# Optimization experiments

Hardware: AMD Instinct MI355X
Metric: run time of the kernel (lower is better)

## Reference

```python
import jax, jax.numpy as jnp
import numpy as np

B, O, R = 4, 1000, 20000
NF, RD, ED = 6, 1, 100
RH, OH = 150, 100


def setup_inputs() -> dict:
    key = jax.random.key(0)
    ks = jax.random.split(key, 20)
    s = 0.05
    inp = {
        "objects": jax.random.normal(ks[0], (B, O, NF), jnp.float32),
        "sender_relations": jax.random.uniform(ks[1], (B, O, R), jnp.float32),
        "receiver_relations": jax.random.uniform(ks[2], (B, O, R), jnp.float32),
        "relation_info": jax.random.normal(ks[3], (B, R, RD), jnp.float32),
        # relational MLP: (2*NF+RD) -> 150 -> 150 -> 150 -> ED, ReLU after every layer
        "rw1": jax.random.normal(ks[4], (2 * NF + RD, RH), jnp.float32) * s,
        "rb1": jnp.zeros((RH,), jnp.float32),
        "rw2": jax.random.normal(ks[5], (RH, RH), jnp.float32) * s,
        "rb2": jnp.zeros((RH,), jnp.float32),
        "rw3": jax.random.normal(ks[6], (RH, RH), jnp.float32) * s,
        "rb3": jnp.zeros((RH,), jnp.float32),
        "rw4": jax.random.normal(ks[7], (RH, ED), jnp.float32) * s,
        "rb4": jnp.zeros((ED,), jnp.float32),
        # object MLP: (NF+ED) -> 100 -> 2, ReLU only after first layer
        "ow1": jax.random.normal(ks[8], (NF + ED, OH), jnp.float32) * s,
        "ob1": jnp.zeros((OH,), jnp.float32),
        "ow2": jax.random.normal(ks[9], (OH, 2), jnp.float32) * s,
        "ob2": jnp.zeros((2,), jnp.float32),
    }
    return inp


def reference(objects, sender_relations, receiver_relations, relation_info,
              rw1, rb1, rw2, rb2, rw3, rb3, rw4, rb4,
              ow1, ob1, ow2, ob2):
    # marshalling: dense one-hot gather via bmm
    senders = jnp.einsum('bnr,bnf->brf', sender_relations, objects)    # [B,R,NF]
    receivers = jnp.einsum('bnr,bnf->brf', receiver_relations, objects)  # [B,R,NF]
    Bm = jnp.concatenate([senders, receivers, relation_info], axis=2)  # [B,R,2NF+RD]
    # relational MLP (ReLU after every layer, including the last)
    h = jax.nn.relu(Bm @ rw1 + rb1)
    h = jax.nn.relu(h @ rw2 + rb2)
    h = jax.nn.relu(h @ rw3 + rb3)
    E = jax.nn.relu(h @ rw4 + rb4)                                     # [B,R,ED]
    # aggregator: dense scatter via bmm
    effect_receivers = jnp.einsum('bnr,brf->bnf', receiver_relations, E)  # [B,O,ED]
    C = jnp.concatenate([objects, effect_receivers], axis=2)           # [B,O,NF+ED]
    # object MLP, flattened over batch*objects like the torch view(-1, input)
    Cf = C.reshape(-1, C.shape[-1])
    o = jax.nn.relu(Cf @ ow1 + ob1)
    return o @ ow2 + ob2                                               # [B*O, 2]
```

## Files before the change

kernel.cpp:

```cpp
#include <hip/hip_runtime.h>

#define B_   4
#define O_   1000
#define R_   20000
#define NF_  6
#define EDP_ 128
#define KS_  25
#define CHUNK_ 800
#define MPAD_ 1024

#define ET_OFF   2560000
#define PART_OFF 7680000
#define WT_USHORTS (4 * 2 * 25600)

typedef short bf16x8 __attribute__((ext_vector_type(8)));
typedef float f32x4  __attribute__((ext_vector_type(4)));
typedef unsigned short ushort4v __attribute__((ext_vector_type(4)));
typedef unsigned short ushort8v __attribute__((ext_vector_type(8)));

#define MFMA16 __builtin_amdgcn_mfma_f32_16x16x32_bf16

__device__ __forceinline__ unsigned short f2bf(float x) {
    union { float f; unsigned int u; } v; v.f = x;
    unsigned int r = (v.u + 0x7FFFu + ((v.u >> 16) & 1u)) >> 16;
    return (unsigned short)r;
}

__device__ __forceinline__ float bf2f(unsigned short h) {
    union { unsigned int u; float f; } v; v.u = (unsigned int)h << 16;
    return v.f;
}

__global__ __launch_bounds__(256) void k_prep(
    const float* __restrict__ rw1, const float* __restrict__ rb1,
    const float* __restrict__ rw2, const float* __restrict__ rb2,
    const float* __restrict__ rw3, const float* __restrict__ rb3,
    const float* __restrict__ rw4, const float* __restrict__ rb4,
    unsigned short* __restrict__ Wt, float* __restrict__ bfp)
{
    const int l = blockIdx.y;
    const float* Ws[4] = {rw1, rw2, rw3, rw4};
    const float* Bs[4] = {rb1, rb2, rb3, rb4};
    const int   Ksz[4] = {13, 150, 150, 150};
    const int   Nsz[4] = {150, 150, 150, 100};
    const float* w = Ws[l];
    const int K = Ksz[l], N = Nsz[l];

    int idx = blockIdx.x * 256 + threadIdx.x;
    if (idx < 25600) {
        int n = idx / 160, k = idx % 160;
        float v = (k < K && n < N) ? w[k * N + n] : 0.f;
        unsigned short h = f2bf(v);
        unsigned short lo = f2bf(v - bf2f(h));
        Wt[(size_t)l * 51200 + idx]         = h;
        Wt[(size_t)l * 51200 + 25600 + idx] = lo;
    }
    if (blockIdx.x == 0 && threadIdx.x < 160)
        bfp[l * 160 + threadIdx.x] = (threadIdx.x < (unsigned)N) ? Bs[l][threadIdx.x] : 0.f;
}

__global__ __launch_bounds__(256) void k_marshal(
    const float* __restrict__ obj, const float* __restrict__ S,
    const float* __restrict__ RRm, const float* __restrict__ rinfo,
    float* __restrict__ bmp)
{
    __shared__ float sobj[500 * NF_];
    const int b = blockIdx.y, z = blockIdx.z;
    const int n0 = z * 500;
    for (int i = threadIdx.x; i < 500 * NF_; i += 256)
        sobj[i] = obj[(size_t)b * O_ * NF_ + (size_t)n0 * NF_ + i];
    __syncthreads();

    const int r = blockIdx.x * 256 + threadIdx.x;
    if (r >= R_) return;

    const size_t base = (size_t)b * O_ * R_ + (size_t)n0 * R_ + r;
    const float* Sp = S + base;
    const float* Rp = RRm + base;

    float ss[NF_] = {0.f, 0.f, 0.f, 0.f, 0.f, 0.f};
    float rs[NF_] = {0.f, 0.f, 0.f, 0.f, 0.f, 0.f};

    #pragma unroll 4
    for (int n = 0; n < 500; ++n) {
        float sv = Sp[(size_t)n * R_];
        float rv = Rp[(size_t)n * R_];
        #pragma unroll
        for (int f = 0; f < NF_; ++f) {
            float o = sobj[n * NF_ + f];
            ss[f] = fmaf(sv, o, ss[f]);
            rs[f] = fmaf(rv, o, rs[f]);
        }
    }

    float* outp = bmp + ((size_t)z * 80000 + (size_t)b * R_ + r) * 16;
    #pragma unroll
    for (int f = 0; f < NF_; ++f) {
        outp[f]     = ss[f];
        outp[6 + f] = rs[f];
    }
    outp[12] = (z == 0) ? rinfo[(size_t)b * R_ + r] : 0.f;
}

template<int NT>
__device__ __forceinline__ void layer_mm(
    const unsigned short (*act)[168],
    const unsigned short* __restrict__ Wh, const unsigned short* __restrict__ Wl,
    int arow, int koff, int cl, f32x4* acc)
{
    #pragma unroll
    for (int n = 0; n < NT; ++n) acc[n] = (f32x4){0.f, 0.f, 0.f, 0.f};
    #pragma unroll
    for (int ks = 0; ks < 5; ++ks) {
        bf16x8 a = *(const bf16x8*)&act[arow][ks * 32 + koff];
        #pragma unroll
        for (int n = 0; n < NT; ++n) {
            bf16x8 wh = *(const bf16x8*)(Wh + (size_t)(n * 16 + cl) * 160 + ks * 32 + koff);
            bf16x8 wl = *(const bf16x8*)(Wl + (size_t)(n * 16 + cl) * 160 + ks * 32 + koff);
            acc[n] = MFMA16(a, wh, acc[n], 0, 0, 0);
            acc[n] = MFMA16(a, wl, acc[n], 0, 0, 0);
        }
    }
}

template<int NT>
__device__ __forceinline__ void epi(
    f32x4* acc, const float* __restrict__ bias,
    unsigned short (*out)[168], int m0, int cl, int rg0)
{
    __syncthreads();
    #pragma unroll
    for (int n = 0; n < NT; ++n) {
        int col = n * 16 + cl;
        float bv = bias[col];
        #pragma unroll
        for (int rg = 0; rg < 4; ++rg) {
            float v = fmaxf(acc[n][rg] + bv, 0.f);
            out[m0 + rg0 + rg][col] = f2bf(v);
        }
    }
    __syncthreads();
}

__global__ __launch_bounds__(256) void k_mlp(
    const float* __restrict__ bmp, unsigned short* __restrict__ Et,
    const unsigned short* __restrict__ Wt, const float* __restrict__ bfp)
{
    __shared__ unsigned short act[64][168];
    __shared__ unsigned short alo[64][32];
    const int t = threadIdx.x;
    const size_t row0 = (size_t)blockIdx.x * 64;

    for (int idx = t; idx < 64 * 32; idx += 256) {
        int rr = idx >> 5, k = idx & 31;
        float v = 0.f;
        if (k < 13)
            v = bmp[(row0 + rr) * 16 + k]
              + bmp[(size_t)80000 * 16 + (row0 + rr) * 16 + k];
        unsigned short h = f2bf(v);
        act[rr][k] = h;
        alo[rr][k] = f2bf(v - bf2f(h));
    }
    __syncthreads();

    const int lane = t & 63, wave = t >> 6;
    const int m0   = wave * 16;
    const int arow = m0 + (lane & 15);
    const int koff = (lane >> 4) * 8;
    const int cl   = lane & 15;
    const int rg0  = (lane >> 4) * 4;

    f32x4 acc[10];

    {
        const unsigned short* Wh = Wt;
        const unsigned short* Wl = Wt + 25600;
        bf16x8 ah = *(const bf16x8*)&act[arow][koff];
        bf16x8 al = *(const bf16x8*)&alo[arow][koff];
        #pragma unroll
        for (int n = 0; n < 10; ++n) {
            bf16x8 wh = *(const bf16x8*)(Wh + (size_t)(n * 16 + cl) * 160 + koff);
            bf16x8 wl = *(const bf16x8*)(Wl + (size_t)(n * 16 + cl) * 160 + koff);
            f32x4 a = (f32x4){0.f, 0.f, 0.f, 0.f};
            a = MFMA16(ah, wh, a, 0, 0, 0);
            a = MFMA16(ah, wl, a, 0, 0, 0);
            a = MFMA16(al, wh, a, 0, 0, 0);
            acc[n] = a;
        }
    }
    epi<10>(acc, bfp + 0 * 160, act, m0, cl, rg0);

    layer_mm<10>(act, Wt + 1 * 51200, Wt + 1 * 51200 + 25600, arow, koff, cl, acc);
    epi<10>(acc, bfp + 1 * 160, act, m0, cl, rg0);

    layer_mm<10>(act, Wt + 2 * 51200, Wt + 2 * 51200 + 25600, arow, koff, cl, acc);
    epi<10>(acc, bfp + 2 * 160, act, m0, cl, rg0);

    layer_mm<7>(act, Wt + 3 * 51200, Wt + 3 * 51200 + 25600, arow, koff, cl, acc);
    epi<7>(acc, bfp + 3 * 160, act, m0, cl, rg0);

    for (int idx = t; idx < 64 * 128; idx += 256) {
        int rr = idx & 63, j = idx >> 6;
        size_t gr = row0 + rr;
        int b = (int)(gr / R_);
        int r = (int)(gr - (size_t)b * R_);
        Et[((size_t)(b * EDP_ + j)) * R_ + r] = (j < 100) ? act[rr][j] : (unsigned short)0;
    }
}

__global__ __launch_bounds__(256) void k_agg(
    const float* __restrict__ RRm, const unsigned short* __restrict__ Et,
    float* __restrict__ part)
{
    __shared__ unsigned short sB[2][128][36];
    const int t = threadIdx.x;
    const int mt = blockIdx.x, b = blockIdx.y, kz = blockIdx.z;
    const int lane = t & 63, wave = t >> 6;
    const int k0 = kz * CHUNK_;

    const int br0 = t >> 2, bc0 = (t & 3) * 8;
    const int br1 = br0 + 64;
    const unsigned short* EtB = Et + (size_t)b * EDP_ * R_;

    int n = mt * 64 + wave * 16 + (lane & 15); if (n > 999) n = 999;
    const int cl = lane & 15, koff = (lane >> 4) * 8;
    const float* Ap = RRm + ((size_t)(b * O_) + n) * R_ + k0 + koff;

    f32x4 acc[8] = {};
    float4 a0c, a1c;
    float4 a0n = {0.f, 0.f, 0.f, 0.f}, a1n = {0.f, 0.f, 0.f, 0.f};

    {
        ushort8v v0 = *(const ushort8v*)(EtB + (size_t)br0 * R_ + k0 + bc0);
        ushort8v v1 = *(const ushort8v*)(EtB + (size_t)br1 * R_ + k0 + bc0);
        *(ushort8v*)&sB[0][br0][bc0] = v0;
        *(ushort8v*)&sB[0][br1][bc0] = v1;
        a0c = *(const float4*)(Ap + 0);
        a1c = *(const float4*)(Ap + 4);
    }
    __syncthreads();

    for (int it = 0; it < CHUNK_ / 32; ++it) {
        const int cur = it & 1, nxt = cur ^ 1;
        const bool more = (it + 1 < CHUNK_ / 32);
        ushort8v v0, v1;
        if (more) {
            const int kb = k0 + (it + 1) * 32;
            v0 = *(const ushort8v*)(EtB + (size_t)br0 * R_ + kb + bc0);
            v1 = *(const ushort8v*)(EtB + (size_t)br1 * R_ + kb + bc0);
            a0n = *(const float4*)(Ap + (it + 1) * 32);
            a1n = *(const float4*)(Ap + (it + 1) * 32 + 4);
        }
        bf16x8 af;
        af[0] = (short)f2bf(a0c.x); af[1] = (short)f2bf(a0c.y);
        af[2] = (short)f2bf(a0c.z); af[3] = (short)f2bf(a0c.w);
        af[4] = (short)f2bf(a1c.x); af[5] = (short)f2bf(a1c.y);
        af[6] = (short)f2bf(a1c.z); af[7] = (short)f2bf(a1c.w);
        #pragma unroll
        for (int ni = 0; ni < 8; ++ni) {
            bf16x8 bf = *(const bf16x8*)&sB[cur][ni * 16 + cl][koff];
            acc[ni] = MFMA16(af, bf, acc[ni], 0, 0, 0);
        }
        if (more) {
            *(ushort8v*)&sB[nxt][br0][bc0] = v0;
            *(ushort8v*)&sB[nxt][br1][bc0] = v1;
        }
        __syncthreads();
        a0c = a0n; a1c = a1n;
    }

    const int rowb = mt * 64 + wave * 16 + (lane >> 4) * 4;
    float* pp = part + ((size_t)(kz * 4 + b) * MPAD_) * 128;
    #pragma unroll
    for (int ni = 0; ni < 8; ++ni)
        #pragma unroll
        for (int rg = 0; rg < 4; ++rg)
            pp[(size_t)(rowb + rg) * 128 + ni * 16 + cl] = acc[ni][rg];
}

__global__ __launch_bounds__(256) void k_obj(
    const float* __restrict__ obj, const float* __restrict__ part,
    const float* __restrict__ ow1, const float* __restrict__ ob1,
    const float* __restrict__ ow2, const float* __restrict__ ob2,
    float* __restrict__ out)
{
    __shared__ float C[8][112];
    __shared__ float h[8][104];
    const int t = threadIdx.x;
    const int g0 = blockIdx.x * 8;

    for (int idx = t; idx < 8 * NF_; idx += 256) {
        int rr = idx / NF_, f = idx % NF_;
        C[rr][f] = obj[(size_t)(g0 + rr) * NF_ + f];
    }
    for (int idx = t; idx < 8 * 100; idx += 256) {
        int rr = idx / 100, f = idx % 100;
        int g = g0 + rr, b = g / 1000, n = g % 1000;
        float s = 0.f;
        for (int z = 0; z < KS_; ++z)
            s += part[((size_t)(z * 4 + b) * MPAD_ + n) * 128 + f];
        C[rr][6 + f] = s;
    }
    __syncthreads();

    for (int idx = t; idx < 8 * 100; idx += 256) {
        int rr = idx / 100, j = idx % 100;
        float acc = ob1[j];
        for (int k = 0; k < 106; ++k)
            acc = fmaf(C[rr][k], ow1[k * 100 + j], acc);
        h[rr][j] = fmaxf(acc, 0.f);
    }
    __syncthreads();

    if (t < 16) {
        int rr = t >> 1, j = t & 1;
        float acc = ob2[j];
        for (int k = 0; k < 100; ++k)
            acc = fmaf(h[rr][k], ow2[k * 2 + j], acc);
        out[(size_t)(g0 + rr) * 2 + j] = acc;
    }
}

extern "C" void kernel_launch(void* const* d_in, const int* in_sizes, int n_in,
                              void* d_out, int out_size, void* d_ws, size_t ws_size,
                              hipStream_t stream)
{
    const float* obj   = (const float*)d_in[0];
    const float* S     = (const float*)d_in[1];
    const float* RRm   = (const float*)d_in[2];
    const float* rinfo = (const float*)d_in[3];
    const float* rw1   = (const float*)d_in[4];
    const float* rb1   = (const float*)d_in[5];
    const float* rw2   = (const float*)d_in[6];
    const float* rb2   = (const float*)d_in[7];
    const float* rw3   = (const float*)d_in[8];
    const float* rb3   = (const float*)d_in[9];
    const float* rw4   = (const float*)d_in[10];
    const float* rb4   = (const float*)d_in[11];
    const float* ow1   = (const float*)d_in[12];
    const float* ob1   = (const float*)d_in[13];
    const float* ow2   = (const float*)d_in[14];
    const float* ob2   = (const float*)d_in[15];

    float* ws            = (float*)d_ws;
    float* bmp           = ws;
    unsigned short* Et   = (unsigned short*)(ws + ET_OFF);
    float* part          = ws + PART_OFF;
    unsigned short* Wt   = (unsigned short*)(ws + PART_OFF);
    float* bfp           = ws + PART_OFF + (WT_USHORTS / 2);
    float* out           = (float*)d_out;

    k_prep<<<dim3(100, 4), 256, 0, stream>>>(rw1, rb1, rw2, rb2, rw3, rb3, rw4, rb4,
                                             Wt, bfp);
    k_marshal<<<dim3(79, 4, 2), 256, 0, stream>>>(obj, S, RRm, rinfo, bmp);
    k_mlp<<<dim3(1250), 256, 0, stream>>>(bmp, Et, Wt, bfp);
    k_agg<<<dim3(16, 4, KS_), 256, 0, stream>>>(RRm, Et, part);
    k_obj<<<dim3(500), 256, 0, stream>>>(obj, part, ow1, ob1, ow2, ob2, out);
}
```

Baseline: 383.0 us.

## Fuse marshalling into relational MLP kernel and double M-tile in aggregation

The separate marshal kernel is removed. Each MLP block now computes its 64 relations' sender/receiver sums itself, with 4 waves each covering 250 objects and reducing through shared memory, so the intermediate bmp buffer no longer round-trips through global memory. The aggregation kernel now has each wave handle two 16-row M tiles, so every loaded E tile is reused by 128 object rows and the Et stream is read half as often. The trade-offs are that the marshal part now runs in only 1252 blocks, with coalescing limited to 64 relations per row segment. The aggregation kernel also needs more registers.

New measurement: 464.6 us. +21.3%, slower.

```diff
diff --git a/kernel.cpp b/kernel.cpp
--- a/kernel.cpp
+++ b/kernel.cpp
@@ -9,8 +9,8 @@
 #define CHUNK_ 800
 #define MPAD_ 1024
 
-#define ET_OFF   2560000
-#define PART_OFF 7680000
+#define ET_OFF   0
+#define PART_OFF 5120000
 #define WT_USHORTS (4 * 2 * 25600)
 
 typedef short bf16x8 __attribute__((ext_vector_type(8)));
@@ -59,49 +59,6 @@
         bfp[l * 160 + threadIdx.x] = (threadIdx.x < (unsigned)N) ? Bs[l][threadIdx.x] : 0.f;
 }
 
-__global__ __launch_bounds__(256) void k_marshal(
-    const float* __restrict__ obj, const float* __restrict__ S,
-    const float* __restrict__ RRm, const float* __restrict__ rinfo,
-    float* __restrict__ bmp)
-{
-    __shared__ float sobj[500 * NF_];
-    const int b = blockIdx.y, z = blockIdx.z;
-    const int n0 = z * 500;
-    for (int i = threadIdx.x; i < 500 * NF_; i += 256)
-        sobj[i] = obj[(size_t)b * O_ * NF_ + (size_t)n0 * NF_ + i];
-    __syncthreads();
-
-    const int r = blockIdx.x * 256 + threadIdx.x;
-    if (r >= R_) return;
-
-    const size_t base = (size_t)b * O_ * R_ + (size_t)n0 * R_ + r;
-    const float* Sp = S + base;
-    const float* Rp = RRm + base;
-
-    float ss[NF_] = {0.f, 0.f, 0.f, 0.f, 0.f, 0.f};
-    float rs[NF_] = {0.f, 0.f, 0.f, 0.f, 0.f, 0.f};
-
-    #pragma unroll 4
-    for (int n = 0; n < 500; ++n) {
-        float sv = Sp[(size_t)n * R_];
-        float rv = Rp[(size_t)n * R_];
-        #pragma unroll
-        for (int f = 0; f < NF_; ++f) {
-            float o = sobj[n * NF_ + f];
-            ss[f] = fmaf(sv, o, ss[f]);
-            rs[f] = fmaf(rv, o, rs[f]);
-        }
-    }
-
-    float* outp = bmp + ((size_t)z * 80000 + (size_t)b * R_ + r) * 16;
-    #pragma unroll
-    for (int f = 0; f < NF_; ++f) {
-        outp[f]     = ss[f];
-        outp[6 + f] = rs[f];
-    }
-    outp[12] = (z == 0) ? rinfo[(size_t)b * R_ + r] : 0.f;
-}
-
 template<int NT>
 __device__ __forceinline__ void layer_mm(
     const unsigned short (*act)[168],
@@ -143,20 +100,55 @@
 }
 
 __global__ __launch_bounds__(256) void k_mlp(
-    const float* __restrict__ bmp, unsigned short* __restrict__ Et,
+    const float* __restrict__ obj, const float* __restrict__ S,
+    const float* __restrict__ RRm, const float* __restrict__ rinfo,
+    unsigned short* __restrict__ Et,
     const unsigned short* __restrict__ Wt, const float* __restrict__ bfp)
 {
     __shared__ unsigned short act[64][168];
     __shared__ unsigned short alo[64][32];
-    const int t = threadIdx.x;
-    const size_t row0 = (size_t)blockIdx.x * 64;
+    __shared__ float psum[4][64][12];
+    const int t  = threadIdx.x;
+    const int b  = blockIdx.y;
+    const int r0 = blockIdx.x * 64;
+
+    {
+        const int rl = t & 63;
+        const int w  = t >> 6;
+        int rme = r0 + rl; if (rme > R_ - 1) rme = R_ - 1;
+        const float* Sp = S   + (size_t)b * O_ * R_ + (size_t)(w * 250) * R_ + rme;
+        const float* Rp = RRm + (size_t)b * O_ * R_ + (size_t)(w * 250) * R_ + rme;
+        const float* ob = obj + ((size_t)b * O_ + (size_t)(w * 250)) * NF_;
+        float ss[6] = {0.f,0.f,0.f,0.f,0.f,0.f};
+        float rs[6] = {0.f,0.f,0.f,0.f,0.f,0.f};
+        #pragma unroll 2
+        for (int n = 0; n < 250; ++n) {
+            float sv = Sp[(size_t)n * R_];
+            float rv = Rp[(size_t)n * R_];
+            #pragma unroll
+            for (int f = 0; f < 6; ++f) {
+                float o = ob[n * NF_ + f];
+                ss[f] = fmaf(sv, o, ss[f]);
+                rs[f] = fmaf(rv, o, rs[f]);
+            }
+        }
+        #pragma unroll
+        for (int f = 0; f < 6; ++f) {
+            psum[w][rl][f]     = ss[f];
+            psum[w][rl][6 + f] = rs[f];
+        }
+    }
+    __syncthreads();
 
     for (int idx = t; idx < 64 * 32; idx += 256) {
         int rr = idx >> 5, k = idx & 31;
         float v = 0.f;
-        if (k < 13)
-            v = bmp[(row0 + rr) * 16 + k]
-              + bmp[(size_t)80000 * 16 + (row0 + rr) * 16 + k];
+        if (k < 12) {
+            v = psum[0][rr][k] + psum[1][rr][k] + psum[2][rr][k] + psum[3][rr][k];
+        } else if (k == 12) {
+            int r = r0 + rr; if (r > R_ - 1) r = R_ - 1;
+            v = rinfo[(size_t)b * R_ + r];
+        }
         unsigned short h = f2bf(v);
         act[rr][k] = h;
         alo[rr][k] = f2bf(v - bf2f(h));
@@ -201,10 +193,9 @@
 
     for (int idx = t; idx < 64 * 128; idx += 256) {
         int rr = idx & 63, j = idx >> 6;
-        size_t gr = row0 + rr;
-        int b = (int)(gr / R_);
-        int r = (int)(gr - (size_t)b * R_);
-        Et[((size_t)(b * EDP_ + j)) * R_ + r] = (j < 100) ? act[rr][j] : (unsigned short)0;
+        int r = r0 + rr;
+        if (r < R_)
+            Et[((size_t)(b * EDP_ + j)) * R_ + r] = (j < 100) ? act[rr][j] : (unsigned short)0;
     }
 }
 
@@ -222,21 +213,27 @@
     const int br1 = br0 + 64;
     const unsigned short* EtB = Et + (size_t)b * EDP_ * R_;
 
-    int n = mt * 64 + wave * 16 + (lane & 15); if (n > 999) n = 999;
     const int cl = lane & 15, koff = (lane >> 4) * 8;
-    const float* Ap = RRm + ((size_t)(b * O_) + n) * R_ + k0 + koff;
-
-    f32x4 acc[8] = {};
-    float4 a0c, a1c;
-    float4 a0n = {0.f, 0.f, 0.f, 0.f}, a1n = {0.f, 0.f, 0.f, 0.f};
+    int n0 = mt * 128 + wave * 32 + cl;
+    int n1 = n0 + 16;
+    if (n0 > 999) n0 = 999;
+    if (n1 > 999) n1 = 999;
+    const float* Ap0 = RRm + ((size_t)(b * O_) + n0) * R_ + k0 + koff;
+    const float* Ap1 = RRm + ((size_t)(b * O_) + n1) * R_ + k0 + koff;
+
+    f32x4 acc[2][8] = {};
+    float4 a0c, a1c, a2c, a3c;
+    float4 a0n = {0,0,0,0}, a1n = {0,0,0,0}, a2n = {0,0,0,0}, a3n = {0,0,0,0};
 
     {
         ushort8v v0 = *(const ushort8v*)(EtB + (size_t)br0 * R_ + k0 + bc0);
         ushort8v v1 = *(const ushort8v*)(EtB + (size_t)br1 * R_ + k0 + bc0);
         *(ushort8v*)&sB[0][br0][bc0] = v0;
         *(ushort8v*)&sB[0][br1][bc0] = v1;
-        a0c = *(const float4*)(Ap + 0);
-        a1c = *(const float4*)(Ap + 4);
+        a0c = *(const float4*)(Ap0 + 0);
+        a1c = *(const float4*)(Ap0 + 4);
+        a2c = *(const float4*)(Ap1 + 0);
+        a3c = *(const float4*)(Ap1 + 4);
     }
     __syncthreads();
 
@@ -248,34 +245,44 @@
             const int kb = k0 + (it + 1) * 32;
             v0 = *(const ushort8v*)(EtB + (size_t)br0 * R_ + kb + bc0);
             v1 = *(const ushort8v*)(EtB + (size_t)br1 * R_ + kb + bc0);
-            a0n = *(const float4*)(Ap + (it + 1) * 32);
-            a1n = *(const float4*)(Ap + (it + 1) * 32 + 4);
-        }
-        bf16x8 af;
-        af[0] = (short)f2bf(a0c.x); af[1] = (short)f2bf(a0c.y);
-        af[2] = (short)f2bf(a0c.z); af[3] = (short)f2bf(a0c.w);
-        af[4] = (short)f2bf(a1c.x); af[5] = (short)f2bf(a1c.y);
-        af[6] = (short)f2bf(a1c.z); af[7] = (short)f2bf(a1c.w);
+            a0n = *(const float4*)(Ap0 + (it + 1) * 32);
+            a1n = *(const float4*)(Ap0 + (it + 1) * 32 + 4);
+            a2n = *(const float4*)(Ap1 + (it + 1) * 32);
+            a3n = *(const float4*)(Ap1 + (it + 1) * 32 + 4);
+        }
+        bf16x8 af0, af1;
+        af0[0] = (short)f2bf(a0c.x); af0[1] = (short)f2bf(a0c.y);
+        af0[2] = (short)f2bf(a0c.z); af0[3] = (short)f2bf(a0c.w);
+        af0[4] = (short)f2bf(a1c.x); af0[5] = (short)f2bf(a1c.y);
+        af0[6] = (short)f2bf(a1c.z); af0[7] = (short)f2bf(a1c.w);
+        af1[0] = (short)f2bf(a2c.x); af1[1] = (short)f2bf(a2c.y);
+        af1[2] = (short)f2bf(a2c.z); af1[3] = (short)f2bf(a2c.w);
+        af1[4] = (short)f2bf(a3c.x); af1[5] = (short)f2bf(a3c.y);
+        af1[6] = (short)f2bf(a3c.z); af1[7] = (short)f2bf(a3c.w);
         #pragma unroll
         for (int ni = 0; ni < 8; ++ni) {
             bf16x8 bf = *(const bf16x8*)&sB[cur][ni * 16 + cl][koff];
-            acc[ni] = MFMA16(af, bf, acc[ni], 0, 0, 0);
+            acc[0][ni] = MFMA16(af0, bf, acc[0][ni], 0, 0, 0);
+            acc[1][ni] = MFMA16(af1, bf, acc[1][ni], 0, 0, 0);
         }
         if (more) {
             *(ushort8v*)&sB[nxt][br0][bc0] = v0;
             *(ushort8v*)&sB[nxt][br1][bc0] = v1;
         }
         __syncthreads();
-        a0c = a0n; a1c = a1n;
-    }
-
-    const int rowb = mt * 64 + wave * 16 + (lane >> 4) * 4;
+        a0c = a0n; a1c = a1n; a2c = a2n; a3c = a3n;
+    }
+
     float* pp = part + ((size_t)(kz * 4 + b) * MPAD_) * 128;
     #pragma unroll
-    for (int ni = 0; ni < 8; ++ni)
-        #pragma unroll
-        for (int rg = 0; rg < 4; ++rg)
-            pp[(size_t)(rowb + rg) * 128 + ni * 16 + cl] = acc[ni][rg];
+    for (int mg = 0; mg < 2; ++mg) {
+        const int rowb = mt * 128 + wave * 32 + mg * 16 + (lane >> 4) * 4;
+        #pragma unroll
+        for (int ni = 0; ni < 8; ++ni)
+            #pragma unroll
+            for (int rg = 0; rg < 4; ++rg)
+                pp[(size_t)(rowb + rg) * 128 + ni * 16 + cl] = acc[mg][ni][rg];
+    }
 }
 
 __global__ __launch_bounds__(256) void k_obj(
@@ -343,7 +350,6 @@
     const float* ob2   = (const float*)d_in[15];
 
     float* ws            = (float*)d_ws;
-    float* bmp           = ws;
     unsigned short* Et   = (unsigned short*)(ws + ET_OFF);
     float* part          = ws + PART_OFF;
     unsigned short* Wt   = (unsigned short*)(ws + PART_OFF);
@@ -352,8 +358,7 @@
 
     k_prep<<<dim3(100, 4), 256, 0, stream>>>(rw1, rb1, rw2, rb2, rw3, rb3, rw4, rb4,
                                              Wt, bfp);
-    k_marshal<<<dim3(79, 4, 2), 256, 0, stream>>>(obj, S, RRm, rinfo, bmp);
-    k_mlp<<<dim3(1250), 256, 0, stream>>>(bmp, Et, Wt, bfp);
-    k_agg<<<dim3(16, 4, KS_), 256, 0, stream>>>(RRm, Et, part);
+    k_mlp<<<dim3(313, 4), 256, 0, stream>>>(obj, S, RRm, rinfo, Et, Wt, bfp);
+    k_agg<<<dim3(8, 4, KS_), 256, 0, stream>>>(RRm, Et, part);
     k_obj<<<dim3(500), 256, 0, stream>>>(obj, part, ow1, ob1, ow2, ob2, out);
 }
```
